# Kernel tuning notes

Measured on AMD Instinct MI355X. Metric: run time of the kernel, lower is better.

The kernel has to match this reference:

```python
import jax, jax.numpy as jnp
import numpy as np

B, C, D, T = 8, 512, 256, 2048
EPS = 1e-5


def setup_inputs() -> dict:
    key = jax.random.key(0)
    ks = jax.random.split(key, 9)
    s_c = 1.0 / np.sqrt(C)
    s_d = 1.0 / np.sqrt(D)
    return {
        "inpt": jax.random.normal(ks[0], (B, C, T), dtype=jnp.float32),
        "theta_w": jax.random.uniform(ks[1], (D, C), jnp.float32, -s_c, s_c),
        "theta_b": jax.random.uniform(ks[2], (D,), jnp.float32, -s_c, s_c),
        "phi_w": jax.random.uniform(ks[3], (D, C), jnp.float32, -s_c, s_c),
        "phi_b": jax.random.uniform(ks[4], (D,), jnp.float32, -s_c, s_c),
        "g_w": jax.random.uniform(ks[5], (D, C), jnp.float32, -s_c, s_c),
        "g_b": jax.random.uniform(ks[6], (D,), jnp.float32, -s_c, s_c),
        "ht_w": jax.random.uniform(ks[7], (C, D), jnp.float32, -s_d, s_d),
        "ht_b": jax.random.uniform(ks[8], (C,), jnp.float32, -s_d, s_d),
        "bn_gamma": jnp.ones((C,), dtype=jnp.float32),
        "bn_beta": jnp.zeros((C,), dtype=jnp.float32),
    }


def reference(inpt, theta_w, theta_b, phi_w, phi_b, g_w, g_b, ht_w, ht_b, bn_gamma, bn_beta):
    # 1x1 convs are just channel-mixing matmuls: (B,C,T) -> (B,D,T)
    theta = jnp.einsum('dc,bct->bdt', theta_w, inpt) + theta_b[None, :, None]
    phi = jnp.einsum('dc,bct->bdt', phi_w, inpt) + phi_b[None, :, None]
    g = jnp.einsum('dc,bct->bdt', g_w, inpt) + g_b[None, :, None]
    # w[b,t,s] = sum_d theta[b,d,t] * phi[b,d,s]; softmax over s (phi time)
    w = jnp.einsum('bdt,bds->bts', theta, phi)
    w = jax.nn.softmax(w, axis=-1)
    # torch.matmul(g, w): out[b,d,s] = sum_t g[b,d,t] * w[b,t,s]
    attn = jnp.einsum('bdt,bts->bds', g, w)
    # ht 1x1 conv back to C channels
    h = jnp.einsum('cd,bdt->bct', ht_w, attn) + ht_b[None, :, None]
    # BatchNorm1d in training mode: batch stats over (B, T) per channel
    mean = jnp.mean(h, axis=(0, 2), keepdims=True)
    var = jnp.var(h, axis=(0, 2), keepdims=True)  # biased variance
    h_norm = (h - mean) * jax.lax.rsqrt(var + EPS)
    bn = bn_gamma[None, :, None] * h_norm + bn_beta[None, :, None]
    return inpt + bn
```

## Files before the change

kernel.cpp:

```cpp
#include <hip/hip_runtime.h>
#include <hip/hip_bf16.h>
#include <math.h>

#define Bx 8
#define Cx 512
#define Dx 256
#define Tx 2048
#define EPSx 1e-5f

typedef _Float16 h16;
typedef __attribute__((ext_vector_type(8))) _Float16 h16x8;
typedef __attribute__((ext_vector_type(8))) short s16x8;
typedef __attribute__((ext_vector_type(4))) float f32x4;

typedef __attribute__((address_space(3))) unsigned int lds_u32;
typedef __attribute__((address_space(1))) const unsigned int glb_u32;

__device__ __forceinline__ void cp16(void* ldsp, const void* g) {
    __builtin_amdgcn_global_load_lds((glb_u32*)g, (lds_u32*)ldsp, 16, 0, 0);
}

template<int MODE, bool BF, int TN>
__global__ __launch_bounds__(256, 4)
void gemm_mf(const h16* __restrict__ A, long aBatch, int lda,
             const h16* __restrict__ B, long bBatch, int ldb,
             void* __restrict__ C, long cBatch, int ldc,
             float* __restrict__ Cp, float* __restrict__ Z,
             int M, int N, int K, int mBlk,
             const float* __restrict__ biasM, const float* __restrict__ biasN) {
    constexpr int NJ = TN / 32;
    __shared__ h16 As[128 * 64];
    __shared__ h16 Bs[TN * 64];
    const int tid  = threadIdx.x;
    const int lane = tid & 63, wid = tid >> 6;
    const int wm = (wid & 1) * 64, wn = (wid >> 1) * (TN / 2);
    const int lm = lane & 15, quad = lane >> 4;
    const unsigned id = blockIdx.x;
    const int b = id & 7;
    const unsigned rr = id >> 3;
    const int m0 = (rr % (unsigned)mBlk) * 128;
    const int n0 = (rr / (unsigned)mBlk) * TN;
    const h16* Ab = A + (size_t)b * aBatch + (size_t)m0 * lda;
    const h16* Bb = B + (size_t)b * bBatch + (size_t)n0 * ldb;

    const int srow  = tid >> 3;
    const int sclog = (tid & 7) ^ (srow & 7);
    char* ldsA = (char*)As + (tid & ~63) * 16;
    char* ldsB = (char*)Bs + (tid & ~63) * 16;

    f32x4 acc[4][NJ] = {};

    for (int k0 = 0; k0 < K; k0 += 64) {
        __syncthreads();
#pragma unroll
        for (int i = 0; i < 4; i++) {
            int r = srow + 32 * i;
            cp16(ldsA + i * 4096, Ab + (size_t)r * lda + k0 + sclog * 8);
        }
#pragma unroll
        for (int i = 0; i < TN / 32; i++) {
            int r = srow + 32 * i;
            cp16(ldsB + i * 4096, Bb + (size_t)r * ldb + k0 + sclog * 8);
        }
        __syncthreads();
#pragma unroll
        for (int ks = 0; ks < 2; ks++) {
            s16x8 af[4], bf4[NJ];
#pragma unroll
            for (int i = 0; i < 4; i++) {
                int row = wm + 16 * i + lm;
                int st = (ks * 4 + quad) ^ (lm & 7);
                af[i] = *(const s16x8*)(As + row * 64 + st * 8);
            }
#pragma unroll
            for (int j = 0; j < NJ; j++) {
                int row = wn + 16 * j + lm;
                int st = (ks * 4 + quad) ^ (lm & 7);
                bf4[j] = *(const s16x8*)(Bs + row * 64 + st * 8);
            }
#pragma unroll
            for (int i = 0; i < 4; i++)
#pragma unroll
                for (int j = 0; j < NJ; j++) {
                    if constexpr (BF)
                        acc[i][j] = __builtin_amdgcn_mfma_f32_16x16x32_bf16(
                            af[i], bf4[j], acc[i][j], 0, 0, 0);
                    else
                        acc[i][j] = __builtin_amdgcn_mfma_f32_16x16x32_f16(
                            __builtin_bit_cast(h16x8, af[i]),
                            __builtin_bit_cast(h16x8, bf4[j]), acc[i][j], 0, 0, 0);
                }
        }
    }

    if constexpr (MODE == 0) {
        h16* Cb = (h16*)C + (size_t)b * cBatch;
#pragma unroll
        for (int i = 0; i < 4; i++)
#pragma unroll
            for (int j = 0; j < NJ; j++) {
                int row = m0 + wm + 16 * i + quad * 4;
                int col = n0 + wn + 16 * j + lm;
                float bN = biasN ? biasN[col] : 0.0f;
#pragma unroll
                for (int r = 0; r < 4; r++) {
                    float v = acc[i][j][r] + bN;
                    if (biasM) v += biasM[row + r];
                    Cb[(size_t)(row + r) * ldc + col] = (h16)v;
                }
            }
    } else if constexpr (MODE == 1) {
        __hip_bfloat16* Cb = (__hip_bfloat16*)C + (size_t)b * cBatch;
#pragma unroll
        for (int j = 0; j < NJ; j++) {
            int col = n0 + wn + 16 * j + lm;
            float iz = 1.0f / Z[(size_t)b * N + col];
#pragma unroll
            for (int i = 0; i < 4; i++) {
                int row = m0 + wm + 16 * i + quad * 4;
#pragma unroll
                for (int r = 0; r < 4; r++) {
                    float v = acc[i][j][r];
                    if (biasM) v += biasM[row + r];
                    Cb[(size_t)(row + r) * ldc + col] = __float2bfloat16(v * iz);
                }
            }
        }
    } else if constexpr (MODE == 2) {
        __syncthreads();
        float* Zl = (float*)As;
        if (tid < TN) Zl[tid] = 0.0f;
        __syncthreads();
        __hip_bfloat16* Cb = (__hip_bfloat16*)C + (size_t)b * cBatch;
#pragma unroll
        for (int j = 0; j < NJ; j++) {
            int cl = wn + 16 * j + lm;
            int col = n0 + cl;
            float zp = 0.0f;
#pragma unroll
            for (int i = 0; i < 4; i++) {
                int row = m0 + wm + 16 * i + quad * 4;
#pragma unroll
                for (int r = 0; r < 4; r++) {
                    float e = __expf(acc[i][j][r]);
                    zp += e;
                    Cb[(size_t)(row + r) * ldc + col] = __float2bfloat16(e);
                }
            }
            atomicAdd(&Zl[cl], zp);
        }
        __syncthreads();
        if (tid < TN) atomicAdd(&Z[(size_t)b * N + n0 + tid], Zl[tid]);
    } else {
        __syncthreads();
        float* Sl = (float*)As;
        float* Sq = Sl + TN;
        if (tid < 2 * TN) Sl[tid] = 0.0f;
        __syncthreads();
        h16* Cb = (h16*)C + (size_t)b * cBatch;
#pragma unroll
        for (int j = 0; j < NJ; j++) {
            int cl = wn + 16 * j + lm;
            int col = n0 + cl;
            float bN = biasN[col];
            float s = 0.0f, q = 0.0f;
#pragma unroll
            for (int i = 0; i < 4; i++) {
                int row = m0 + wm + 16 * i + quad * 4;
#pragma unroll
                for (int r = 0; r < 4; r++) {
                    float v = acc[i][j][r] + bN;
                    s += v;
                    q = fmaf(v, v, q);
                    Cb[(size_t)(row + r) * ldc + col] = (h16)v;
                }
            }
            atomicAdd(&Sl[cl], s);
            atomicAdd(&Sq[cl], q);
        }
        __syncthreads();
        if (tid < TN) {
            atomicAdd(&Cp[n0 + tid], Sl[tid]);
            atomicAdd(&Z[n0 + tid], Sq[tid]);
        }
    }
}

__global__ __launch_bounds__(256)
void conv_prep(const float* __restrict__ inpt, h16* __restrict__ xT,
               const float* __restrict__ w0, const float* __restrict__ w1,
               const float* __restrict__ w2, const float* __restrict__ w3,
               const float* __restrict__ tb, const float* __restrict__ pb,
               const float* __restrict__ gb,
               h16* __restrict__ dst, float* __restrict__ bias3,
               float* __restrict__ Z, float* __restrict__ psum,
               float* __restrict__ pssq) {
    const int tid = threadIdx.x;
    if (blockIdx.z == 8) {
        int bx = blockIdx.y * 32 + blockIdx.x;
#pragma unroll
        for (int rep = 0; rep < 2; rep++) {
            int idx4 = bx * 512 + rep * 256 + tid;
            int arr = idx4 >> 15, local4 = idx4 & 32767;
            const float* srcs[4] = {w0, w1, w2, w3};
            float4 v = ((const float4*)srcs[arr])[local4];
            h16 o[4] = {(h16)v.x, (h16)v.y, (h16)v.z, (h16)v.w};
            *(uint2*)(dst + (size_t)arr * 131072 + (size_t)local4 * 4) = *(uint2*)o;
        }
        if (bx < 64) Z[bx * 256 + tid] = 0.0f;
        if (bx == 64) bias3[tid] = tb[tid];
        if (bx == 65) bias3[256 + tid] = pb[tid];
        if (bx == 66) bias3[512 + tid] = gb[tid];
        if (bx == 67) {
            psum[tid] = 0.0f; psum[tid + 256] = 0.0f;
            pssq[tid] = 0.0f; pssq[tid + 256] = 0.0f;
        }
        return;
    }
    __shared__ float lds[64][68];
    const int b = blockIdx.z;
    const int t0 = blockIdx.x * 64, c0 = blockIdx.y * 64;
    const int q = tid >> 4, k = tid & 15;
    const float* ib = inpt + (size_t)b * Cx * Tx;
#pragma unroll
    for (int i = 0; i < 4; i++) {
        int c = q + 16 * i;
        float4 v = *(const float4*)(ib + (size_t)(c0 + c) * Tx + t0 + 4 * k);
        *(float4*)&lds[c][4 * k] = v;
    }
    __syncthreads();
    h16* xb = xT + (size_t)b * Tx * Cx;
#pragma unroll
    for (int i = 0; i < 4; i++) {
        int t = q + 16 * i;
        h16 o[4];
#pragma unroll
        for (int j = 0; j < 4; j++) o[j] = (h16)lds[4 * k + j][t];
        *(uint2*)(xb + (size_t)(t0 + t) * Cx + c0 + 4 * k) = *(uint2*)o;
    }
}

__global__ __launch_bounds__(256)
void bn_apply_T(const float* __restrict__ inpt, const h16* __restrict__ hT,
                const float* __restrict__ psum, const float* __restrict__ pssq,
                const float* __restrict__ gamma, const float* __restrict__ beta,
                float* __restrict__ out) {
    __shared__ float lds[64][68];
    const int b = blockIdx.z, t0 = blockIdx.x * 64, c0 = blockIdx.y * 64;
    const int tid = threadIdx.x, q = tid >> 4, k = tid & 15;
    const h16* hb = hT + (size_t)b * Tx * Cx;
#pragma unroll
    for (int i = 0; i < 4; i++) {
        int t = q + 16 * i;
        uint2 raw = *(const uint2*)(hb + (size_t)(t0 + t) * Cx + c0 + 4 * k);
        const h16* hp = (const h16*)&raw;
        float4 v = make_float4((float)hp[0], (float)hp[1], (float)hp[2], (float)hp[3]);
        *(float4*)&lds[t][4 * k] = v;
    }
    __syncthreads();
    const float* ib = inpt + (size_t)b * Cx * Tx;
    float* ob = out + (size_t)b * Cx * Tx;
    const float invN = 1.0f / (float)(Bx * Tx);
#pragma unroll
    for (int i = 0; i < 4; i++) {
        int c = q + 16 * i;
        int cg = c0 + c;
        float mu = psum[cg] * invN;
        float var = pssq[cg] * invN - mu * mu;
        float rv = rsqrtf(var + EPSx);
        float ga = gamma[cg], be = beta[cg];
        float4 x = *(const float4*)(ib + (size_t)cg * Tx + t0 + 4 * k);
        float4 o;
        o.x = x.x + ga * (lds[4 * k + 0][c] - mu) * rv + be;
        o.y = x.y + ga * (lds[4 * k + 1][c] - mu) * rv + be;
        o.z = x.z + ga * (lds[4 * k + 2][c] - mu) * rv + be;
        o.w = x.w + ga * (lds[4 * k + 3][c] - mu) * rv + be;
        *(float4*)(ob + (size_t)cg * Tx + t0 + 4 * k) = o;
    }
}

extern "C" void kernel_launch(void* const* d_in, const int* in_sizes, int n_in,
                              void* d_out, int out_size, void* d_ws, size_t ws_size,
                              hipStream_t stream) {
    const float* inpt    = (const float*)d_in[0];
    const float* theta_w = (const float*)d_in[1];
    const float* theta_b = (const float*)d_in[2];
    const float* phi_w   = (const float*)d_in[3];
    const float* phi_b   = (const float*)d_in[4];
    const float* g_w     = (const float*)d_in[5];
    const float* g_b     = (const float*)d_in[6];
    const float* ht_w    = (const float*)d_in[7];
    const float* ht_b    = (const float*)d_in[8];
    const float* gamma   = (const float*)d_in[9];
    const float* beta    = (const float*)d_in[10];

    char* ws = (char*)d_ws;
    h16*   xT    = (h16*)(ws + 0);
    h16*   w4    = (h16*)(ws + 16777216);
    h16*   wHt   = w4 + 393216;
    float* bias3 = (float*)(ws + 17825792);
    float* Z     = (float*)(ws + 17828864);
    float* psum  = (float*)(ws + 17894400);
    float* pssq  = (float*)(ws + 17896448);
    h16*   thph  = (h16*)(ws + 17902592);
    h16*   gT    = (h16*)(ws + 34679808);
    h16*   attn  = (h16*)(ws + 43068416);
    h16*   LT    = (h16*)(ws + 51457024);
    h16*   hT    = xT;

    const long sX  = (long)Tx * Cx;
    const long sTP = (long)Tx * 512;
    const long sGT = (long)Dx * Tx;
    const long sAT = (long)Tx * Dx;
    const long sW  = (long)Tx * Tx;

    dim3 blk(256);
    conv_prep<<<dim3(Tx / 64, Cx / 64, Bx + 1), blk, 0, stream>>>(
        inpt, xT, theta_w, phi_w, g_w, ht_w, theta_b, phi_b, g_b,
        w4, bias3, Z, psum, pssq);
    gemm_mf<0, false, 128><<<dim3(512), blk, 0, stream>>>(
        xT, sX, Cx, w4, 0, Cx, thph, sTP, 512, nullptr, nullptr,
        Tx, 512, Cx, 16, nullptr, bias3);
    gemm_mf<2, false, 128><<<dim3(2048), blk, 0, stream>>>(
        thph + 256, sTP, 512, thph, sTP, 512, LT, sW, Tx, nullptr, Z,
        Tx, Tx, Dx, 16, nullptr, nullptr);
    gemm_mf<1, false, 64><<<dim3(512), blk, 0, stream>>>(
        w4 + 512 * 512, 0, Cx, xT, sX, Cx, gT, sGT, Tx, nullptr, Z,
        Dx, Tx, Cx, 2, bias3 + 512, nullptr);
    gemm_mf<0, true, 64><<<dim3(512), blk, 0, stream>>>(
        LT, sW, Tx, gT, sGT, Tx, attn, sAT, Dx, nullptr, nullptr,
        Tx, Dx, Tx, 16, nullptr, nullptr);
    gemm_mf<3, false, 64><<<dim3(1024), blk, 0, stream>>>(
        attn, sAT, Dx, wHt, 0, Dx, hT, sX, Cx, psum, pssq,
        Tx, Cx, Dx, 16, nullptr, ht_b);
    bn_apply_T<<<dim3(Tx / 64, Cx / 64, Bx), blk, 0, stream>>>(
        inpt, hT, psum, pssq, gamma, beta, (float*)d_out);
}
```

Before: 216.8 us.

## Double-buffer LDS staging in GEMMs and read fp16 residual in BN apply

Adds a double-buffered LDS path to the MFMA GEMM so the next K tile's global-to-LDS copy overlaps the current tile's MFMAs, with one barrier per iteration; enabled for all GEMMs except the large L=theta^T phi one. The BN apply kernel now reads the residual from the fp16 transposed input copy rather than the fp32 input, and hoists per-channel statistics. hT moves to its own workspace region so xT stays intact. Doubling LDS may reduce occupancy, and the fp16 residual adds rounding error to the output.

Measured after the change: 231.2 us. 6.6% more time.

```diff
diff --git a/kernel.cpp b/kernel.cpp
--- a/kernel.cpp
+++ b/kernel.cpp
@@ -20,7 +20,7 @@
     __builtin_amdgcn_global_load_lds((glb_u32*)g, (lds_u32*)ldsp, 16, 0, 0);
 }
 
-template<int MODE, bool BF, int TN>
+template<int MODE, bool BF, int TN, bool DBUF>
 __global__ __launch_bounds__(256, 4)
 void gemm_mf(const h16* __restrict__ A, long aBatch, int lda,
              const h16* __restrict__ B, long bBatch, int ldb,
@@ -29,8 +29,9 @@
              int M, int N, int K, int mBlk,
              const float* __restrict__ biasM, const float* __restrict__ biasN) {
     constexpr int NJ = TN / 32;
-    __shared__ h16 As[128 * 64];
-    __shared__ h16 Bs[TN * 64];
+    constexpr int NB = DBUF ? 2 : 1;
+    __shared__ h16 As[NB * 128 * 64];
+    __shared__ h16 Bs[NB * TN * 64];
     const int tid  = threadIdx.x;
     const int lane = tid & 63, wid = tid >> 6;
     const int wm = (wid & 1) * 64, wn = (wid >> 1) * (TN / 2);
@@ -45,24 +46,26 @@
 
     const int srow  = tid >> 3;
     const int sclog = (tid & 7) ^ (srow & 7);
-    char* ldsA = (char*)As + (tid & ~63) * 16;
-    char* ldsB = (char*)Bs + (tid & ~63) * 16;
 
     f32x4 acc[4][NJ] = {};
 
-    for (int k0 = 0; k0 < K; k0 += 64) {
-        __syncthreads();
+    auto stage = [&](int buf, int k0) {
+        char* lA = (char*)As + buf * 16384 + (tid & ~63) * 16;
+        char* lB = (char*)Bs + buf * (TN * 128) + (tid & ~63) * 16;
 #pragma unroll
         for (int i = 0; i < 4; i++) {
             int r = srow + 32 * i;
-            cp16(ldsA + i * 4096, Ab + (size_t)r * lda + k0 + sclog * 8);
+            cp16(lA + i * 4096, Ab + (size_t)r * lda + k0 + sclog * 8);
         }
 #pragma unroll
         for (int i = 0; i < TN / 32; i++) {
             int r = srow + 32 * i;
-            cp16(ldsB + i * 4096, Bb + (size_t)r * ldb + k0 + sclog * 8);
-        }
-        __syncthreads();
+            cp16(lB + i * 4096, Bb + (size_t)r * ldb + k0 + sclog * 8);
+        }
+    };
+    auto compute = [&](int buf) {
+        const h16* Ac = As + buf * (128 * 64);
+        const h16* Bc = Bs + buf * (TN * 64);
 #pragma unroll
         for (int ks = 0; ks < 2; ks++) {
             s16x8 af[4], bf4[NJ];
@@ -70,13 +73,13 @@
             for (int i = 0; i < 4; i++) {
                 int row = wm + 16 * i + lm;
                 int st = (ks * 4 + quad) ^ (lm & 7);
-                af[i] = *(const s16x8*)(As + row * 64 + st * 8);
+                af[i] = *(const s16x8*)(Ac + row * 64 + st * 8);
             }
 #pragma unroll
             for (int j = 0; j < NJ; j++) {
                 int row = wn + 16 * j + lm;
                 int st = (ks * 4 + quad) ^ (lm & 7);
-                bf4[j] = *(const s16x8*)(Bs + row * 64 + st * 8);
+                bf4[j] = *(const s16x8*)(Bc + row * 64 + st * 8);
             }
 #pragma unroll
             for (int i = 0; i < 4; i++)
@@ -90,6 +93,27 @@
                             __builtin_bit_cast(h16x8, af[i]),
                             __builtin_bit_cast(h16x8, bf4[j]), acc[i][j], 0, 0, 0);
                 }
+        }
+    };
+
+    if constexpr (!DBUF) {
+        for (int k0 = 0; k0 < K; k0 += 64) {
+            __syncthreads();
+            stage(0, k0);
+            __syncthreads();
+            compute(0);
+        }
+    } else {
+        stage(0, 0);
+        asm volatile("s_waitcnt vmcnt(0)" ::: "memory");
+        __builtin_amdgcn_s_barrier();
+        int cur = 0;
+        for (int k0 = 0; k0 < K; k0 += 64) {
+            if (k0 + 64 < K) stage(cur ^ 1, k0 + 64);
+            compute(cur);
+            asm volatile("s_waitcnt vmcnt(0)" ::: "memory");
+            __builtin_amdgcn_s_barrier();
+            cur ^= 1;
         }
     }
 
@@ -241,40 +265,52 @@
 }
 
 __global__ __launch_bounds__(256)
-void bn_apply_T(const float* __restrict__ inpt, const h16* __restrict__ hT,
+void bn_apply_T(const h16* __restrict__ xT, const h16* __restrict__ hT,
                 const float* __restrict__ psum, const float* __restrict__ pssq,
                 const float* __restrict__ gamma, const float* __restrict__ beta,
                 float* __restrict__ out) {
     __shared__ float lds[64][68];
     const int b = blockIdx.z, t0 = blockIdx.x * 64, c0 = blockIdx.y * 64;
     const int tid = threadIdx.x, q = tid >> 4, k = tid & 15;
+    const float invN = 1.0f / (float)(Bx * Tx);
+    float mu[4], rv[4], ga[4], be[4];
+#pragma unroll
+    for (int j = 0; j < 4; j++) {
+        int cg = c0 + 4 * k + j;
+        float m = psum[cg] * invN;
+        float var = pssq[cg] * invN - m * m;
+        mu[j] = m;
+        rv[j] = rsqrtf(var + EPSx);
+        ga[j] = gamma[cg];
+        be[j] = beta[cg];
+    }
     const h16* hb = hT + (size_t)b * Tx * Cx;
+    const h16* xb = xT + (size_t)b * Tx * Cx;
 #pragma unroll
     for (int i = 0; i < 4; i++) {
         int t = q + 16 * i;
-        uint2 raw = *(const uint2*)(hb + (size_t)(t0 + t) * Cx + c0 + 4 * k);
-        const h16* hp = (const h16*)&raw;
-        float4 v = make_float4((float)hp[0], (float)hp[1], (float)hp[2], (float)hp[3]);
-        *(float4*)&lds[t][4 * k] = v;
+        size_t off = (size_t)(t0 + t) * Cx + c0 + 4 * k;
+        uint2 hraw = *(const uint2*)(hb + off);
+        uint2 xraw = *(const uint2*)(xb + off);
+        const h16* hp = (const h16*)&hraw;
+        const h16* xp = (const h16*)&xraw;
+        float o[4];
+#pragma unroll
+        for (int j = 0; j < 4; j++)
+            o[j] = (float)xp[j] + ga[j] * ((float)hp[j] - mu[j]) * rv[j] + be[j];
+        *(float4*)&lds[t][4 * k] = *(float4*)o;
     }
     __syncthreads();
-    const float* ib = inpt + (size_t)b * Cx * Tx;
     float* ob = out + (size_t)b * Cx * Tx;
-    const float invN = 1.0f / (float)(Bx * Tx);
 #pragma unroll
     for (int i = 0; i < 4; i++) {
         int c = q + 16 * i;
         int cg = c0 + c;
-        float mu = psum[cg] * invN;
-        float var = pssq[cg] * invN - mu * mu;
-        float rv = rsqrtf(var + EPSx);
-        float ga = gamma[cg], be = beta[cg];
-        float4 x = *(const float4*)(ib + (size_t)cg * Tx + t0 + 4 * k);
         float4 o;
-        o.x = x.x + ga * (lds[4 * k + 0][c] - mu) * rv + be;
-        o.y = x.y + ga * (lds[4 * k + 1][c] - mu) * rv + be;
-        o.z = x.z + ga * (lds[4 * k + 2][c] - mu) * rv + be;
-        o.w = x.w + ga * (lds[4 * k + 3][c] - mu) * rv + be;
+        o.x = lds[4 * k + 0][c];
+        o.y = lds[4 * k + 1][c];
+        o.z = lds[4 * k + 2][c];
+        o.w = lds[4 * k + 3][c];
         *(float4*)(ob + (size_t)cg * Tx + t0 + 4 * k) = o;
     }
 }
@@ -306,7 +342,7 @@
     h16*   gT    = (h16*)(ws + 34679808);
     h16*   attn  = (h16*)(ws + 43068416);
     h16*   LT    = (h16*)(ws + 51457024);
-    h16*   hT    = xT;
+    h16*   hT    = (h16*)(ws + 118565888);
 
     const long sX  = (long)Tx * Cx;
     const long sTP = (long)Tx * 512;
@@ -318,21 +354,21 @@
     conv_prep<<<dim3(Tx / 64, Cx / 64, Bx + 1), blk, 0, stream>>>(
         inpt, xT, theta_w, phi_w, g_w, ht_w, theta_b, phi_b, g_b,
         w4, bias3, Z, psum, pssq);
-    gemm_mf<0, false, 128><<<dim3(512), blk, 0, stream>>>(
+    gemm_mf<0, false, 128, true><<<dim3(512), blk, 0, stream>>>(
         xT, sX, Cx, w4, 0, Cx, thph, sTP, 512, nullptr, nullptr,
         Tx, 512, Cx, 16, nullptr, bias3);
-    gemm_mf<2, false, 128><<<dim3(2048), blk, 0, stream>>>(
+    gemm_mf<2, false, 128, false><<<dim3(2048), blk, 0, stream>>>(
         thph + 256, sTP, 512, thph, sTP, 512, LT, sW, Tx, nullptr, Z,
         Tx, Tx, Dx, 16, nullptr, nullptr);
-    gemm_mf<1, false, 64><<<dim3(512), blk, 0, stream>>>(
+    gemm_mf<1, false, 64, true><<<dim3(512), blk, 0, stream>>>(
         w4 + 512 * 512, 0, Cx, xT, sX, Cx, gT, sGT, Tx, nullptr, Z,
         Dx, Tx, Cx, 2, bias3 + 512, nullptr);
-    gemm_mf<0, true, 64><<<dim3(512), blk, 0, stream>>>(
+    gemm_mf<0, true, 64, true><<<dim3(512), blk, 0, stream>>>(
         LT, sW, Tx, gT, sGT, Tx, attn, sAT, Dx, nullptr, nullptr,
         Tx, Dx, Tx, 16, nullptr, nullptr);
-    gemm_mf<3, false, 64><<<dim3(1024), blk, 0, stream>>>(
+    gemm_mf<3, false, 64, true><<<dim3(1024), blk, 0, stream>>>(
         attn, sAT, Dx, wHt, 0, Dx, hT, sX, Cx, psum, pssq,
         Tx, Cx, Dx, 16, nullptr, ht_b);
     bn_apply_T<<<dim3(Tx / 64, Cx / 64, Bx), blk, 0, stream>>>(
-        inpt, hT, psum, pssq, gamma, beta, (float*)d_out);
-}
+        xT, hT, psum, pssq, gamma, beta, (float*)d_out);
+}
```
